# Optimization experiments

Measured on AMD Instinct MI355X. Metric: run time of the kernel, lower is better.

## Reference

```python
import jax, jax.numpy as jnp
import numpy as np

N_GROUP = 8
TOPK_GROUP = 4
TOP_K = 8
ROUTED_SCALING_FACTOR = 2.5
RENORMALIZE = True


def setup_inputs() -> dict:
    key = jax.random.key(0)
    k1, k2 = jax.random.split(key)
    num_tokens, n_experts = 131072, 256
    router_logits = jax.random.normal(k1, (num_tokens, n_experts), dtype=jnp.float32)
    e_score_correction_bias = jax.random.normal(k2, (n_experts,), dtype=jnp.float32) * 0.1
    return {"router_logits": router_logits,
            "e_score_correction_bias": e_score_correction_bias}


def reference(router_logits, e_score_correction_bias):
    T, E = router_logits.shape
    per_group = E // N_GROUP  # 32 experts per group

    # sigmoid scoring + bias correction (bias used for selection only)
    scores = jax.nn.sigmoid(router_logits)                      # [T, E]
    scores_for_choice = scores + e_score_correction_bias[None, :]

    # group score = sum of top-2 corrected scores within each group
    grouped = scores_for_choice.reshape(T, N_GROUP, per_group)  # [T, G, E/G]
    top2_vals, _ = jax.lax.top_k(grouped, 2)                    # [T, G, 2]
    group_scores = top2_vals.sum(axis=-1)                       # [T, G]

    # pick topk_group groups, build expert-level mask
    _, group_idx = jax.lax.top_k(group_scores, TOPK_GROUP)      # [T, topk_group]
    group_mask = jnp.zeros((T, N_GROUP), dtype=jnp.bool_)
    group_mask = group_mask.at[jnp.arange(T)[:, None], group_idx].set(True)
    score_mask = jnp.repeat(group_mask, per_group, axis=1)      # [T, E]

    # mask non-selected groups, then global top-k over remaining experts
    masked_scores = jnp.where(score_mask, scores_for_choice, 0.0)
    _, topk_ids = jax.lax.top_k(masked_scores, TOP_K)           # [T, top_k]

    # gather UNcorrected sigmoid scores as weights
    topk_weights = jnp.take_along_axis(scores, topk_ids, axis=1)  # [T, top_k]
    if RENORMALIZE:
        topk_weights = topk_weights / (topk_weights.sum(axis=-1, keepdims=True) + 1e-20)
    topk_weights = topk_weights * ROUTED_SCALING_FACTOR
    return topk_weights, topk_ids
```

## Files before the change

### kernel.cpp

```cpp
#include <hip/hip_runtime.h>
#include <math.h>

#define THREADS 256
#define TPB 32
#define NEXP 256
#define EPS_G 4.0e-6f
#define Q_EPS 9u

__device__ __forceinline__ float fsigmoid(float x) {
    float e = __expf(-x);
    return __fdividef(1.0f, 1.0f + e);
}

__device__ __forceinline__ double dsigmoid(float xf) {
    xf = fminf(fmaxf(xf, -500.0f), 500.0f);
    double x = (double)xf;
    double t = x * -1.4426950408889634074;
    double n = floor(t + 0.5);
    int ni = (int)n;
    double u = (t - n) * 0.69314718055994530942;
    double pp = 2.08767569878680990e-9;
    pp = fma(pp, u, 2.50521083854417188e-8);
    pp = fma(pp, u, 2.75573192239858907e-7);
    pp = fma(pp, u, 2.75573192239858883e-6);
    pp = fma(pp, u, 2.48015873015873016e-5);
    pp = fma(pp, u, 1.98412698412698413e-4);
    pp = fma(pp, u, 1.38888888888888889e-3);
    pp = fma(pp, u, 8.33333333333333333e-3);
    pp = fma(pp, u, 4.16666666666666667e-2);
    pp = fma(pp, u, 1.66666666666666667e-1);
    pp = fma(pp, u, 0.5);
    pp = fma(pp, u, 1.0);
    pp = fma(pp, u, 1.0);
    double sc = __longlong_as_double((long long)(1023 + ni) << 52);
    double e = pp * sc;
    double w = 1.0 + e;
    double y = (double)__fdividef(1.0f, (float)w);
    y = fma(y, fma(-w, y, 1.0), y);
    y = fma(y, fma(-w, y, 1.0), y);
    return y;
}

#define DINS(cc, ee) do {                                                \
    double _d=(cc); int _e=(ee);                                         \
    if (_d > s7) {                                                       \
        bool _b0=_d>s0,_b1=_d>s1,_b2=_d>s2,_b3=_d>s3,_b4=_d>s4,          \
             _b5=_d>s5,_b6=_d>s6;                                        \
        s7=_b6?s6:_d;           c7=_b6?c6:_e;                            \
        s6=_b5?s5:(_b6?_d:s6);  c6=_b5?c5:(_b6?_e:c6);                   \
        s5=_b4?s4:(_b5?_d:s5);  c5=_b4?c4:(_b5?_e:c5);                   \
        s4=_b3?s3:(_b4?_d:s4);  c4=_b3?c3:(_b4?_e:c4);                   \
        s3=_b2?s2:(_b3?_d:s3);  c3=_b2?c2:(_b3?_e:c3);                   \
        s2=_b1?s1:(_b2?_d:s2);  c2=_b1?c1:(_b2?_e:c2);                   \
        s1=_b0?s0:(_b1?_d:s1);  c1=_b0?c0:(_b1?_e:c1);                   \
        s0=_b0?_d:s0;           c0=_b0?_e:c0;                            \
    } } while (0)

__device__ __forceinline__ unsigned pack_key(float c, unsigned idflip) {
    unsigned q = (unsigned)fmaf(c, 4194304.0f, 2097152.0f);
    return (q << 8) + idflip;
}

#define CEU(a, b) do {                                                   \
    unsigned _x=(a), _y=(b);                                             \
    (a) = _x>_y ? _x : _y; (b) = _x>_y ? _y : _x;                        \
} while (0)
#define VMU(a, b) do { (a) = (a)>(b) ? (a) : (b); } while (0)

#define SORT8U(v0,v1,v2,v3,v4,v5,v6,v7) do {                             \
    CEU(v0,v1); CEU(v2,v3); CEU(v4,v5); CEU(v6,v7);                      \
    CEU(v0,v2); CEU(v1,v3); CEU(v4,v6); CEU(v5,v7);                      \
    CEU(v1,v2); CEU(v5,v6);                                              \
    CEU(v0,v4); CEU(v1,v5); CEU(v2,v6); CEU(v3,v7);                      \
    CEU(v2,v4); CEU(v3,v5);                                              \
    CEU(v1,v2); CEU(v3,v4); CEU(v5,v6);                                  \
} while (0)

#define CLEAN9U do {                                                     \
    CEU(m0,m8);                                                          \
    CEU(m1,m5); CEU(m2,m6); CEU(m3,m7); CEU(m4,m8);                      \
    CEU(m1,m3); CEU(m2,m4); CEU(m5,m7); CEU(m6,m8);                      \
    CEU(m1,m2); CEU(m3,m4); CEU(m5,m6); CEU(m7,m8);                      \
} while (0)

#define XMERGE_U(d) do {                                                 \
    unsigned q0=(unsigned)__shfl_xor((int)m0,d,64),                      \
             q1=(unsigned)__shfl_xor((int)m1,d,64),                      \
             q2=(unsigned)__shfl_xor((int)m2,d,64),                      \
             q3=(unsigned)__shfl_xor((int)m3,d,64),                      \
             q4=(unsigned)__shfl_xor((int)m4,d,64),                      \
             q5=(unsigned)__shfl_xor((int)m5,d,64),                      \
             q6=(unsigned)__shfl_xor((int)m6,d,64),                      \
             q7=(unsigned)__shfl_xor((int)m7,d,64),                      \
             q8=(unsigned)__shfl_xor((int)m8,d,64);                      \
    VMU(m0,q8); VMU(m1,q7); VMU(m2,q6); VMU(m3,q5); VMU(m4,q4);          \
    VMU(m5,q3); VMU(m6,q2); VMU(m7,q1); VMU(m8,q0);                      \
    CLEAN9U;                                                             \
} while (0)

__device__ __forceinline__ float4 shfl4(float4 v, int src) {
    float4 r;
    r.x = __shfl(v.x, src, 64);
    r.y = __shfl(v.y, src, 64);
    r.z = __shfl(v.z, src, 64);
    r.w = __shfl(v.w, src, 64);
    return r;
}

__global__ __launch_bounds__(THREADS, 4)
void noauxtc_router_kernel(const float* __restrict__ logits,
                           const float* __restrict__ bias,
                           float* __restrict__ out,
                           int T)
{
    __shared__ __align__(16) float bias_sh[NEXP];

    const int tid   = threadIdx.x;
    const int h     = tid & 7;
    const int p     = tid >> 3;
    const int tok0  = blockIdx.x * TPB;
    const int token = tok0 + p;
    const int lane  = tid & 63;
    const int base  = lane & 56;

    const float4* lg4 = (const float4*)logits;
    float4 st[8];
    #pragma unroll
    for (int k = 0; k < 8; ++k)
        st[k] = lg4[(size_t)token * 64 + h * 8 + k];

    bias_sh[tid] = bias[tid];
    __syncthreads();

    const float4* bias4 = (const float4*)bias_sh;

    float g1 = -3e38f, g2 = -3e38f;
    #pragma unroll
    for (int q = 0; q < 8; ++q) {
        float4 bb = bias4[h * 8 + q];
        float4 c;
        c.x = fsigmoid(st[q].x) + bb.x;
        c.y = fsigmoid(st[q].y) + bb.y;
        c.z = fsigmoid(st[q].z) + bb.z;
        c.w = fsigmoid(st[q].w) + bb.w;
        st[q] = c;
        float h1 = fmaxf(c.x, c.y), l1 = fminf(c.x, c.y);
        float h2 = fmaxf(c.z, c.w), l2 = fminf(c.z, c.w);
        float t1 = fmaxf(h1, h2);
        float t2 = fmaxf(fminf(h1, h2), fmaxf(l1, l2));
        g2 = fmaxf(fminf(g1, t1), fmaxf(g2, t2));
        g1 = fmaxf(g1, t1);
    }
    float gs = g1 + g2;

    float gsv[8];
    #pragma unroll
    for (int g = 0; g < 8; ++g) gsv[g] = __shfl(gs, base + g, 64);

    int selmask = 0; float val4 = 0.f, val5 = 0.f;
    #pragma unroll
    for (int a = 0; a < 8; ++a) {
        int rk = 0;
        #pragma unroll
        for (int b = 0; b < 8; ++b) {
            if (b == a) continue;
            bool beat = (b < a) ? (gsv[b] >= gsv[a]) : (gsv[b] > gsv[a]);
            rk += beat ? 1 : 0;
        }
        selmask |= (rk < 4) ? (1 << a) : 0;
        val4 = (rk == 3) ? gsv[a] : val4;
        val5 = (rk == 4) ? gsv[a] : val5;
    }

    if (__builtin_expect(val4 - val5 < EPS_G, 0)) {
        double a1 = -1e300, a2 = -1e300;
        const float* lgp = logits + (size_t)token * 256 + h * 32;
        #pragma unroll 1
        for (int k = 0; k < 32; ++k) {
            double c = dsigmoid(lgp[k]) + (double)bias_sh[h * 32 + k];
            a2 = fmax(a2, fmin(a1, c)); a1 = fmax(a1, c);
        }
        double gdo = a1 + a2;
        double gd[8];
        #pragma unroll
        for (int g = 0; g < 8; ++g) gd[g] = __shfl(gdo, base + g, 64);
        int sm = 0;
        #pragma unroll
        for (int a = 0; a < 8; ++a) {
            int rk = 0;
            #pragma unroll
            for (int b = 0; b < 8; ++b) {
                if (b == a) continue;
                bool beat = (b < a) ? (gd[b] >= gd[a]) : (gd[b] > gd[a]);
                rk += beat ? 1 : 0;
            }
            sm |= (rk < 4) ? (1 << a) : 0;
        }
        selmask = sm;
    }

    const int want = h >> 1;
    int g = 0, cnt = 0;
    #pragma unroll
    for (int a = 0; a < 8; ++a) {
        bool s = (selmask >> a) & 1;
        g = (s && (cnt == want)) ? a : g;
        cnt += s ? 1 : 0;
    }
    const int hf  = h & 1;
    const int src = base + g;

    float4 ga[4];
    #pragma unroll
    for (int j = 0; j < 4; ++j) {
        float4 t0 = shfl4(st[j],     src);
        float4 t1 = shfl4(st[j + 4], src);
        ga[j] = hf ? t1 : t0;
    }

    const int ebase = g * 32 + hf * 16;
    const unsigned idf = 255u - (unsigned)ebase;

    unsigned k0=pack_key(ga[0].x, idf-0),  k1=pack_key(ga[0].y, idf-1),
             k2=pack_key(ga[0].z, idf-2),  k3=pack_key(ga[0].w, idf-3),
             k4=pack_key(ga[1].x, idf-4),  k5=pack_key(ga[1].y, idf-5),
             k6=pack_key(ga[1].z, idf-6),  k7=pack_key(ga[1].w, idf-7);
    unsigned l0=pack_key(ga[2].x, idf-8),  l1=pack_key(ga[2].y, idf-9),
             l2=pack_key(ga[2].z, idf-10), l3=pack_key(ga[2].w, idf-11),
             l4=pack_key(ga[3].x, idf-12), l5=pack_key(ga[3].y, idf-13),
             l6=pack_key(ga[3].z, idf-14), l7=pack_key(ga[3].w, idf-15);

    SORT8U(k0,k1,k2,k3,k4,k5,k6,k7);
    SORT8U(l0,l1,l2,l3,l4,l5,l6,l7);

    unsigned m0=k0, m1=k1, m2=k2, m3=k3, m4=k4, m5=k5, m6=k6, m7=k7, m8=0u;
    VMU(m1,l7); VMU(m2,l6); VMU(m3,l5); VMU(m4,l4);
    VMU(m5,l3); VMU(m6,l2); VMU(m7,l1); VMU(m8,l0);
    CLEAN9U;

    XMERGE_U(1);
    XMERGE_U(2);
    XMERGE_U(4);

    unsigned q0=m0>>8, q1=m1>>8, q2=m2>>8, q3=m3>>8, q4=m4>>8,
             q5=m5>>8, q6=m6>>8, q7=m7>>8, q8=m8>>8;
    int n0=255-(int)(m0&255u), n1=255-(int)(m1&255u), n2=255-(int)(m2&255u),
        n3=255-(int)(m3&255u), n4=255-(int)(m4&255u), n5=255-(int)(m5&255u),
        n6=255-(int)(m6&255u), n7=255-(int)(m7&255u), n8=255-(int)(m8&255u);

    const float QS = 2.384185791015625e-7f;
    float v0=(float)q0*QS-0.5f, v1=(float)q1*QS-0.5f, v2=(float)q2*QS-0.5f,
          v3=(float)q3*QS-0.5f, v4=(float)q4*QS-0.5f, v5=(float)q5*QS-0.5f,
          v6=(float)q6*QS-0.5f, v7=(float)q7*QS-0.5f;

    float w0 = v0 - bias_sh[n0], w1 = v1 - bias_sh[n1], w2 = v2 - bias_sh[n2],
          w3 = v3 - bias_sh[n3], w4 = v4 - bias_sh[n4], w5 = v5 - bias_sh[n5],
          w6 = v6 - bias_sh[n6], w7 = v7 - bias_sh[n7];
    int o0=n0,o1=n1,o2=n2,o3=n3,o4=n4,o5=n5,o6=n6,o7=n7;

    bool flagB = (h == 0) &&
                 ((q0-q1<Q_EPS)|(q1-q2<Q_EPS)|(q2-q3<Q_EPS)|(q3-q4<Q_EPS)|
                  (q4-q5<Q_EPS)|(q5-q6<Q_EPS)|(q6-q7<Q_EPS)|(q7-q8<Q_EPS));
    if (__builtin_expect(flagB, 0)) {
        double s0=-1e300,s1=-1e300,s2=-1e300,s3=-1e300,
               s4=-1e300,s5=-1e300,s6=-1e300,s7=-1e300;
        int c0=0,c1=0,c2=0,c3=0,c4=0,c5=0,c6=0,c7=0;
        int ci[9] = {n0,n1,n2,n3,n4,n5,n6,n7,n8};
        const float* lgt = logits + (size_t)token * 256;
        #pragma unroll 1
        for (int k = 0; k < 9; ++k) {
            int e = ci[k];
            double cs = dsigmoid(lgt[e]) + (double)bias_sh[e];
            DINS(cs, e);
        }
        w0=(float)(s0-(double)bias_sh[c0]); o0=c0;
        w1=(float)(s1-(double)bias_sh[c1]); o1=c1;
        w2=(float)(s2-(double)bias_sh[c2]); o2=c2;
        w3=(float)(s3-(double)bias_sh[c3]); o3=c3;
        w4=(float)(s4-(double)bias_sh[c4]); o4=c4;
        w5=(float)(s5-(double)bias_sh[c5]); o5=c5;
        w6=(float)(s6-(double)bias_sh[c6]); o6=c6;
        w7=(float)(s7-(double)bias_sh[c7]); o7=c7;
    }

    if (h == 0) {
        float sum = ((w0+w1)+(w2+w3)) + ((w4+w5)+(w6+w7));
        float scl = 2.5f / (sum + 1e-20f);
        float4 oa, ob;
        oa.x=w0*scl; oa.y=w1*scl; oa.z=w2*scl; oa.w=w3*scl;
        ob.x=w4*scl; ob.y=w5*scl; ob.z=w6*scl; ob.w=w7*scl;
        *(float4*)(out + (size_t)token*8)     = oa;
        *(float4*)(out + (size_t)token*8 + 4) = ob;
        float* oid = out + (size_t)T*8;
        float4 ia, ib;
        ia.x=(float)o0; ia.y=(float)o1; ia.z=(float)o2; ia.w=(float)o3;
        ib.x=(float)o4; ib.y=(float)o5; ib.z=(float)o6; ib.w=(float)o7;
        *(float4*)(oid + (size_t)token*8)     = ia;
        *(float4*)(oid + (size_t)token*8 + 4) = ib;
    }
}

extern "C" void kernel_launch(void* const* d_in, const int* in_sizes, int n_in,
                              void* d_out, int out_size, void* d_ws, size_t ws_size,
                              hipStream_t stream) {
    const float* logits = (const float*)d_in[0];
    const float* bias   = (const float*)d_in[1];
    float* out = (float*)d_out;
    int T = in_sizes[0] / NEXP;
    int nblocks = T / TPB;
    noauxtc_router_kernel<<<nblocks, THREADS, 0, stream>>>(logits, bias, out, T);
}
```

Measured before the change: 198.0 us.

## Compute per-group top-9 once on packed keys and reuse for group scoring

Each thread now packs its 32 corrected scores into quantized integer keys (with bias pre-quantized in shared memory), sorts them, and builds a top-9 list that gives both the group score (top two keys) and the candidates for the final merge. This removes the float group-score pass and the register shuffles that redistributed selected groups' scores across lanes. Unselected groups' lists are zeroed before the xor-merge. The exchange is more sorting work per thread (four 8-sorts plus merges) and a quantized group-score tie threshold, which risks different tie handling and needs a retuned fallback epsilon.

After: 200.6 us. No clear change (+1.3%).

```diff
diff --git a/kernel.cpp b/kernel.cpp
--- a/kernel.cpp
+++ b/kernel.cpp
@@ -4,8 +4,8 @@
 #define THREADS 256
 #define TPB 32
 #define NEXP 256
-#define EPS_G 4.0e-6f
-#define Q_EPS 9u
+#define Q_EPS  12u
+#define QG_EPS 28u
 
 __device__ __forceinline__ float fsigmoid(float x) {
     float e = __expf(-x);
@@ -56,10 +56,6 @@
         s0=_b0?_d:s0;           c0=_b0?_e:c0;                            \
     } } while (0)
 
-__device__ __forceinline__ unsigned pack_key(float c, unsigned idflip) {
-    unsigned q = (unsigned)fmaf(c, 4194304.0f, 2097152.0f);
-    return (q << 8) + idflip;
-}
 
 #define CEU(a, b) do {                                                   \
     unsigned _x=(a), _y=(b);                                             \
@@ -76,11 +72,11 @@
     CEU(v1,v2); CEU(v3,v4); CEU(v5,v6);                                  \
 } while (0)
 
-#define CLEAN9U do {                                                     \
-    CEU(m0,m8);                                                          \
-    CEU(m1,m5); CEU(m2,m6); CEU(m3,m7); CEU(m4,m8);                      \
-    CEU(m1,m3); CEU(m2,m4); CEU(m5,m7); CEU(m6,m8);                      \
-    CEU(m1,m2); CEU(m3,m4); CEU(m5,m6); CEU(m7,m8);                      \
+#define CLEAN9M(a0,a1,a2,a3,a4,a5,a6,a7,a8) do {                         \
+    CEU(a0,a8);                                                          \
+    CEU(a1,a5); CEU(a2,a6); CEU(a3,a7); CEU(a4,a8);                      \
+    CEU(a1,a3); CEU(a2,a4); CEU(a5,a7); CEU(a6,a8);                      \
+    CEU(a1,a2); CEU(a3,a4); CEU(a5,a6); CEU(a7,a8);                      \
 } while (0)
 
 #define XMERGE_U(d) do {                                                 \
@@ -95,17 +91,8 @@
              q8=(unsigned)__shfl_xor((int)m8,d,64);                      \
     VMU(m0,q8); VMU(m1,q7); VMU(m2,q6); VMU(m3,q5); VMU(m4,q4);          \
     VMU(m5,q3); VMU(m6,q2); VMU(m7,q1); VMU(m8,q0);                      \
-    CLEAN9U;                                                             \
-} while (0)
-
-__device__ __forceinline__ float4 shfl4(float4 v, int src) {
-    float4 r;
-    r.x = __shfl(v.x, src, 64);
-    r.y = __shfl(v.y, src, 64);
-    r.z = __shfl(v.z, src, 64);
-    r.w = __shfl(v.w, src, 64);
-    return r;
-}
+    CLEAN9M(m0,m1,m2,m3,m4,m5,m6,m7,m8);                                 \
+} while (0)
 
 __global__ __launch_bounds__(THREADS, 4)
 void noauxtc_router_kernel(const float* __restrict__ logits,
@@ -114,6 +101,7 @@
                            int T)
 {
     __shared__ __align__(16) float bias_sh[NEXP];
+    __shared__ __align__(16) float biasq_sh[NEXP];
 
     const int tid   = threadIdx.x;
     const int h     = tid & 7;
@@ -129,50 +117,64 @@
     for (int k = 0; k < 8; ++k)
         st[k] = lg4[(size_t)token * 64 + h * 8 + k];
 
-    bias_sh[tid] = bias[tid];
+    {
+        float b = bias[tid];
+        bias_sh[tid]  = b;
+        biasq_sh[tid] = fmaf(b, 4194304.0f, 2097152.0f);
+    }
     __syncthreads();
 
-    const float4* bias4 = (const float4*)bias_sh;
-
-    float g1 = -3e38f, g2 = -3e38f;
+    const float4* bq4 = (const float4*)biasq_sh;
+
+    unsigned kk[32];
     #pragma unroll
     for (int q = 0; q < 8; ++q) {
-        float4 bb = bias4[h * 8 + q];
-        float4 c;
-        c.x = fsigmoid(st[q].x) + bb.x;
-        c.y = fsigmoid(st[q].y) + bb.y;
-        c.z = fsigmoid(st[q].z) + bb.z;
-        c.w = fsigmoid(st[q].w) + bb.w;
-        st[q] = c;
-        float h1 = fmaxf(c.x, c.y), l1 = fminf(c.x, c.y);
-        float h2 = fmaxf(c.z, c.w), l2 = fminf(c.z, c.w);
-        float t1 = fmaxf(h1, h2);
-        float t2 = fmaxf(fminf(h1, h2), fmaxf(l1, l2));
-        g2 = fmaxf(fminf(g1, t1), fmaxf(g2, t2));
-        g1 = fmaxf(g1, t1);
-    }
-    float gs = g1 + g2;
-
-    float gsv[8];
-    #pragma unroll
-    for (int g = 0; g < 8; ++g) gsv[g] = __shfl(gs, base + g, 64);
-
-    int selmask = 0; float val4 = 0.f, val5 = 0.f;
-    #pragma unroll
-    for (int a = 0; a < 8; ++a) {
-        int rk = 0;
-        #pragma unroll
-        for (int b = 0; b < 8; ++b) {
-            if (b == a) continue;
-            bool beat = (b < a) ? (gsv[b] >= gsv[a]) : (gsv[b] > gsv[a]);
-            rk += beat ? 1 : 0;
-        }
-        selmask |= (rk < 4) ? (1 << a) : 0;
-        val4 = (rk == 3) ? gsv[a] : val4;
-        val5 = (rk == 4) ? gsv[a] : val5;
-    }
-
-    if (__builtin_expect(val4 - val5 < EPS_G, 0)) {
+        float4 Bq = bq4[h * 8 + q];
+        float4 x  = st[q];
+        int idf = 255 - (h * 32 + q * 4);
+        kk[q*4+0] = ((unsigned)fmaf(fsigmoid(x.x), 4194304.0f, Bq.x) << 8) + (unsigned)(idf    );
+        kk[q*4+1] = ((unsigned)fmaf(fsigmoid(x.y), 4194304.0f, Bq.y) << 8) + (unsigned)(idf - 1);
+        kk[q*4+2] = ((unsigned)fmaf(fsigmoid(x.z), 4194304.0f, Bq.z) << 8) + (unsigned)(idf - 2);
+        kk[q*4+3] = ((unsigned)fmaf(fsigmoid(x.w), 4194304.0f, Bq.w) << 8) + (unsigned)(idf - 3);
+    }
+
+    SORT8U(kk[0], kk[1], kk[2], kk[3], kk[4], kk[5], kk[6], kk[7]);
+    SORT8U(kk[8], kk[9], kk[10],kk[11],kk[12],kk[13],kk[14],kk[15]);
+    SORT8U(kk[16],kk[17],kk[18],kk[19],kk[20],kk[21],kk[22],kk[23]);
+    SORT8U(kk[24],kk[25],kk[26],kk[27],kk[28],kk[29],kk[30],kk[31]);
+
+    unsigned t0=kk[0],t1=kk[1],t2=kk[2],t3=kk[3],t4=kk[4],t5=kk[5],t6=kk[6],t7=kk[7],t8=0u;
+    VMU(t1,kk[15]); VMU(t2,kk[14]); VMU(t3,kk[13]); VMU(t4,kk[12]);
+    VMU(t5,kk[11]); VMU(t6,kk[10]); VMU(t7,kk[9]);  VMU(t8,kk[8]);
+    CLEAN9M(t0,t1,t2,t3,t4,t5,t6,t7,t8);
+
+    unsigned u0=kk[16],u1=kk[17],u2=kk[18],u3=kk[19],u4=kk[20],u5=kk[21],u6=kk[22],u7=kk[23],u8=0u;
+    VMU(u1,kk[31]); VMU(u2,kk[30]); VMU(u3,kk[29]); VMU(u4,kk[28]);
+    VMU(u5,kk[27]); VMU(u6,kk[26]); VMU(u7,kk[25]); VMU(u8,kk[24]);
+    CLEAN9M(u0,u1,u2,u3,u4,u5,u6,u7,u8);
+
+    unsigned m0=t0,m1=t1,m2=t2,m3=t3,m4=t4,m5=t5,m6=t6,m7=t7,m8=t8;
+    VMU(m0,u8); VMU(m1,u7); VMU(m2,u6); VMU(m3,u5); VMU(m4,u4);
+    VMU(m5,u3); VMU(m6,u2); VMU(m7,u1); VMU(m8,u0);
+    CLEAN9M(m0,m1,m2,m3,m4,m5,m6,m7,m8);
+
+    unsigned gq   = (m0 >> 8) + (m1 >> 8);
+    unsigned gkey = (gq << 3) + (unsigned)(7 - h);
+
+    unsigned gk0 = (unsigned)__shfl((int)gkey, base + 0, 64);
+    unsigned gk1 = (unsigned)__shfl((int)gkey, base + 1, 64);
+    unsigned gk2 = (unsigned)__shfl((int)gkey, base + 2, 64);
+    unsigned gk3 = (unsigned)__shfl((int)gkey, base + 3, 64);
+    unsigned gk4 = (unsigned)__shfl((int)gkey, base + 4, 64);
+    unsigned gk5 = (unsigned)__shfl((int)gkey, base + 5, 64);
+    unsigned gk6 = (unsigned)__shfl((int)gkey, base + 6, 64);
+    unsigned gk7 = (unsigned)__shfl((int)gkey, base + 7, 64);
+    SORT8U(gk0,gk1,gk2,gk3,gk4,gk5,gk6,gk7);
+
+    int selmask = (1 << ((gk0 & 7u) ^ 7u)) | (1 << ((gk1 & 7u) ^ 7u)) |
+                  (1 << ((gk2 & 7u) ^ 7u)) | (1 << ((gk3 & 7u) ^ 7u));
+
+    if (__builtin_expect((gk3 >> 3) - (gk4 >> 3) < QG_EPS, 0)) {
         double a1 = -1e300, a2 = -1e300;
         const float* lgp = logits + (size_t)token * 256 + h * 32;
         #pragma unroll 1
@@ -199,44 +201,12 @@
         selmask = sm;
     }
 
-    const int want = h >> 1;
-    int g = 0, cnt = 0;
-    #pragma unroll
-    for (int a = 0; a < 8; ++a) {
-        bool s = (selmask >> a) & 1;
-        g = (s && (cnt == want)) ? a : g;
-        cnt += s ? 1 : 0;
-    }
-    const int hf  = h & 1;
-    const int src = base + g;
-
-    float4 ga[4];
-    #pragma unroll
-    for (int j = 0; j < 4; ++j) {
-        float4 t0 = shfl4(st[j],     src);
-        float4 t1 = shfl4(st[j + 4], src);
-        ga[j] = hf ? t1 : t0;
-    }
-
-    const int ebase = g * 32 + hf * 16;
-    const unsigned idf = 255u - (unsigned)ebase;
-
-    unsigned k0=pack_key(ga[0].x, idf-0),  k1=pack_key(ga[0].y, idf-1),
-             k2=pack_key(ga[0].z, idf-2),  k3=pack_key(ga[0].w, idf-3),
-             k4=pack_key(ga[1].x, idf-4),  k5=pack_key(ga[1].y, idf-5),
-             k6=pack_key(ga[1].z, idf-6),  k7=pack_key(ga[1].w, idf-7);
-    unsigned l0=pack_key(ga[2].x, idf-8),  l1=pack_key(ga[2].y, idf-9),
-             l2=pack_key(ga[2].z, idf-10), l3=pack_key(ga[2].w, idf-11),
-             l4=pack_key(ga[3].x, idf-12), l5=pack_key(ga[3].y, idf-13),
-             l6=pack_key(ga[3].z, idf-14), l7=pack_key(ga[3].w, idf-15);
-
-    SORT8U(k0,k1,k2,k3,k4,k5,k6,k7);
-    SORT8U(l0,l1,l2,l3,l4,l5,l6,l7);
-
-    unsigned m0=k0, m1=k1, m2=k2, m3=k3, m4=k4, m5=k5, m6=k6, m7=k7, m8=0u;
-    VMU(m1,l7); VMU(m2,l6); VMU(m3,l5); VMU(m4,l4);
-    VMU(m5,l3); VMU(m6,l2); VMU(m7,l1); VMU(m8,l0);
-    CLEAN9U;
+    {
+        bool sel = (selmask >> h) & 1;
+        m0 = sel ? m0 : 0u; m1 = sel ? m1 : 0u; m2 = sel ? m2 : 0u;
+        m3 = sel ? m3 : 0u; m4 = sel ? m4 : 0u; m5 = sel ? m5 : 0u;
+        m6 = sel ? m6 : 0u; m7 = sel ? m7 : 0u; m8 = sel ? m8 : 0u;
+    }
 
     XMERGE_U(1);
     XMERGE_U(2);
```
